# Kernel optimization log

Measured on AMD Instinct MI355X. Metric: run time of the kernel, lower is better.

Reference implementation:

```python
import jax, jax.numpy as jnp
import numpy as np
from jax import lax

T, D, H, O = 16384, 257, 512, 257


def setup_inputs() -> dict:
    key = jax.random.key(0)
    ks = jax.random.split(key, 7)
    s = 1.0 / np.sqrt(H)  # PyTorch LSTM/Linear uniform init scale
    u = lambda k, shp: jax.random.uniform(k, shp, jnp.float32, -s, s)
    return {
        "stft": jax.random.normal(ks[0], (T, D), jnp.float32),
        "W_ih": u(ks[1], (4 * H, D)),
        "W_hh": u(ks[2], (4 * H, H)),
        "b_ih": u(ks[3], (4 * H,)),
        "b_hh": u(ks[4], (4 * H,)),
        "W_out": u(ks[5], (O, H)),
        "b_out": u(ks[6], (O,)),
    }


def reference(stft, W_ih, W_hh, b_ih, b_hh, W_out, b_out):
    # Batch size is 1 (stft.view(T, 1, -1)), so we scan over [T, D] directly.
    # Precompute input-to-gate GEMM for all timesteps: [T, 4H]
    x_gates = stft @ W_ih.T + (b_ih + b_hh)

    def step(carry, xg):
        h, c = carry  # [H], [H]
        g = xg + h @ W_hh.T  # [4H], PyTorch gate order: i, f, g, o
        i, f, gg, o = jnp.split(g, 4)
        i = jax.nn.sigmoid(i)
        f = jax.nn.sigmoid(f)
        gg = jnp.tanh(gg)
        o = jax.nn.sigmoid(o)
        c = f * c + i * gg
        h = o * jnp.tanh(c)
        return (h, c), h

    h0 = jnp.zeros((H,), stft.dtype)  # init_hidden(): zeros
    c0 = jnp.zeros((H,), stft.dtype)
    _, hs = lax.scan(step, (h0, c0), x_gates)  # hs: [T, H]

    out_space = hs @ W_out.T + b_out  # [T, O]
    return jax.nn.log_softmax(out_space, axis=1)
```

## Files before the change

kernel.cpp:

```cpp
#include <hip/hip_runtime.h>
#include <cmath>

#define T_STEPS 16384
#define D_IN    257
#define H_DIM   512
#define O_DIM   257
#define G4      2048

typedef unsigned long long u64;

#define WS_XG_OFF     8192
#define WS_HS_OFF     (8192 + (size_t)T_STEPS * G4 * 4)

__device__ inline float fast_sigmoid(float x) {
    return 1.f / (1.f + __expf(-x));
}
__device__ inline float fast_tanh(float x) {
    float ax = fminf(fabsf(x), 15.f);
    float e  = __expf(2.f * ax);
    float t  = (e - 1.f) / (e + 1.f);
    return copysignf(t, x);
}
__device__ inline float dot4(float4 a, float4 b) {
    return a.x * b.x + a.y * b.y + a.z * b.z + a.w * b.w;
}

#define PIN4(v) asm volatile("" : "+v"(v.x), "+v"(v.y), "+v"(v.z), "+v"(v.w))

__global__ __launch_bounds__(256) void xgate_gemm(
    const float* __restrict__ stft, const float* __restrict__ W_ih,
    const float* __restrict__ b_ih, const float* __restrict__ b_hh,
    float* __restrict__ xg)
{
    const int tid = threadIdx.x;
    const int tx = tid & 15, ty = tid >> 4;
    const int j0 = blockIdx.x * 64;
    const int t0 = blockIdx.y * 64;

    __shared__ float s_a[64][17];
    __shared__ float s_b[64][17];

    float acc[4][4] = {};

    for (int k0 = 0; k0 < D_IN; k0 += 16) {
        #pragma unroll
        for (int l = 0; l < 4; ++l) {
            int idx = tid + l * 256;
            int r  = idx >> 4;
            int kk = idx & 15;
            int k  = k0 + kk;
            s_a[r][kk] = (k < D_IN) ? stft[(size_t)(t0 + r) * D_IN + k] : 0.f;
            s_b[r][kk] = (k < D_IN) ? W_ih[(size_t)(j0 + r) * D_IN + k] : 0.f;
        }
        __syncthreads();
        #pragma unroll
        for (int kk = 0; kk < 16; ++kk) {
            float a[4], b[4];
            #pragma unroll
            for (int r = 0; r < 4; ++r) a[r] = s_a[ty * 4 + r][kk];
            #pragma unroll
            for (int c = 0; c < 4; ++c) b[c] = s_b[tx * 4 + c][kk];
            #pragma unroll
            for (int r = 0; r < 4; ++r)
                #pragma unroll
                for (int c = 0; c < 4; ++c)
                    acc[r][c] += a[r] * b[c];
        }
        __syncthreads();
    }

    float bias[4];
    #pragma unroll
    for (int c = 0; c < 4; ++c) {
        int j = j0 + tx * 4 + c;
        bias[c] = b_ih[j] + b_hh[j];
    }
    #pragma unroll
    for (int r = 0; r < 4; ++r) {
        int t = t0 + ty * 4 + r;
        #pragma unroll
        for (int c = 0; c < 4; ++c) {
            xg[(size_t)t * G4 + j0 + tx * 4 + c] = acc[r][c] + bias[c];
        }
    }
}

__global__ __launch_bounds__(512, 1) void lstm_seq(
    const float* __restrict__ W_hh, const float* __restrict__ xg,
    float* __restrict__ hs, u64* __restrict__ msg)
{
    const int tid  = threadIdx.x;
    const int g    = blockIdx.x;
    const int w    = tid >> 6;
    const int lane = tid & 63;
    const int j    = lane >> 2;
    const int c    = lane & 3;
    const int colb = w * 64 + c * 16;

    const float* wbase = W_hh + (size_t)(g * 16 + j) * H_DIM + colb;
    const size_t gstride = (size_t)H_DIM * H_DIM;
    float4 wA0, wA1, wA2, wA3, wB0, wB1, wB2, wB3;
    float4 wC0, wC1, wC2, wC3, wD0, wD1, wD2, wD3;
    {
        const float4* p0 = (const float4*)(wbase);
        const float4* p1 = (const float4*)(wbase + gstride);
        const float4* p2 = (const float4*)(wbase + 2 * gstride);
        const float4* p3 = (const float4*)(wbase + 3 * gstride);
        wA0 = p0[0]; wA1 = p0[1]; wA2 = p0[2]; wA3 = p0[3];
        wB0 = p1[0]; wB1 = p1[1]; wB2 = p1[2]; wB3 = p1[3];
        wC0 = p2[0]; wC1 = p2[1]; wC2 = p2[2]; wC3 = p2[3];
        wD0 = p3[0]; wD1 = p3[1]; wD2 = p3[2]; wD3 = p3[3];
    }
    PIN4(wA0); PIN4(wA1); PIN4(wA2); PIN4(wA3);
    PIN4(wB0); PIN4(wB1); PIN4(wB2); PIN4(wB3);
    PIN4(wC0); PIN4(wC1); PIN4(wC2); PIN4(wC3);
    PIN4(wD0); PIN4(wD1); PIN4(wD2); PIN4(wD3);

    __shared__ float s_h[512];
    __shared__ float s_part[2][512];

    u64* slot0 = msg;
    u64* slot1 = msg + 512;

    float c_state = 0.f;
    const int t_j = lane & 15;

    for (int t = 0; t < T_STEPS; ++t) {
        const unsigned tagt = (unsigned)t;
        const int buf = t & 1;

        float xv = 0.f;
        if (w == 0)
            xv = __builtin_nontemporal_load(
                xg + (size_t)t * G4 + (lane >> 4) * H_DIM + g * 16 + t_j);

        u64* rp = (buf ? slot1 : slot0) + tid;
        u64 a0 = __hip_atomic_load(rp, __ATOMIC_RELAXED, __HIP_MEMORY_SCOPE_AGENT);
        u64 a1 = __hip_atomic_load(rp, __ATOMIC_RELAXED, __HIP_MEMORY_SCOPE_AGENT);
        u64 a2 = __hip_atomic_load(rp, __ATOMIC_RELAXED, __HIP_MEMORY_SCOPE_AGENT);
        while ((unsigned)(a0 >> 32) != tagt) {
            a0 = a1;
            a1 = a2;
            a2 = __hip_atomic_load(rp, __ATOMIC_RELAXED, __HIP_MEMORY_SCOPE_AGENT);
        }
        const u64 u = a0;

        s_h[tid] = __uint_as_float((unsigned)u);

        const float4* hv = (const float4*)(s_h + colb);
        float4 h0 = hv[0], h1 = hv[1], h2 = hv[2], h3 = hv[3];

        float p0 = dot4(wA0, h0) + dot4(wA1, h1) + dot4(wA2, h2) + dot4(wA3, h3);
        float p1 = dot4(wB0, h0) + dot4(wB1, h1) + dot4(wB2, h2) + dot4(wB3, h3);
        float p2 = dot4(wC0, h0) + dot4(wC1, h1) + dot4(wC2, h2) + dot4(wC3, h3);
        float p3 = dot4(wD0, h0) + dot4(wD1, h1) + dot4(wD2, h2) + dot4(wD3, h3);

        const bool lo2 = (c < 2);
        float a0f = (lo2 ? p0 : p2) + __shfl_xor(lo2 ? p2 : p0, 2, 64);
        float a1f = (lo2 ? p1 : p3) + __shfl_xor(lo2 ? p3 : p1, 2, 64);
        const bool ev = ((c & 1) == 0);
        float fin = (ev ? a0f : a1f) + __shfl_xor(ev ? a1f : a0f, 1, 64);

        s_part[buf][w * 64 + c * 16 + j] = fin;

        asm volatile("s_waitcnt lgkmcnt(0)\n\ts_barrier" ::: "memory");

        if (w == 0) {
            const float* pp = &s_part[buf][0];
            float sum = xv;
            #pragma unroll
            for (int k = 0; k < 8; ++k) sum += pp[k * 64 + lane];

            float gi = __shfl(sum, t_j + 0,  64);
            float gf = __shfl(sum, t_j + 16, 64);
            float gg = __shfl(sum, t_j + 32, 64);
            float go = __shfl(sum, t_j + 48, 64);

            float iv = fast_sigmoid(gi);
            float fv = fast_sigmoid(gf);
            float ov = fast_sigmoid(go);
            float gv = fast_tanh(gg);
            c_state = fv * c_state + iv * gv;
            float hn = ov * fast_tanh(c_state);

            if (lane < 16) {
                __builtin_nontemporal_store(hn, hs + (size_t)t * H_DIM + g * 16 + lane);
                u64 m = ((u64)(tagt + 1) << 32) | (u64)__float_as_uint(hn);
                u64* wp = (((t + 1) & 1) ? slot1 : slot0) + (g * 16 + lane);
                __hip_atomic_store(wp, m, __ATOMIC_RELAXED, __HIP_MEMORY_SCOPE_AGENT);
            }
        }
    }
}

__global__ __launch_bounds__(256) void out_softmax(
    const float* __restrict__ hs, const float* __restrict__ W_out,
    const float* __restrict__ b_out, float* __restrict__ out)
{
    const int tid = threadIdx.x;
    const int t0  = blockIdx.x * 16;

    __shared__ float s_w[257 * 33];
    __shared__ float s_hs[16 * 33];
    __shared__ float s_o[16 * 257];
    __shared__ float s_red[8];

    float acc[16] = {};
    float acc256 = 0.f;

    for (int k0 = 0; k0 < H_DIM; k0 += 32) {
        for (int idx = tid; idx < 257 * 32; idx += 256) {
            int row = idx >> 5, col = idx & 31;
            s_w[row * 33 + col] = W_out[(size_t)row * H_DIM + k0 + col];
        }
        for (int idx = tid; idx < 16 * 32; idx += 256) {
            int row = idx >> 5, col = idx & 31;
            s_hs[row * 33 + col] = hs[(size_t)(t0 + row) * H_DIM + k0 + col];
        }
        __syncthreads();
        #pragma unroll
        for (int kk = 0; kk < 32; ++kk) {
            float w = s_w[tid * 33 + kk];
            #pragma unroll
            for (int r = 0; r < 16; ++r)
                acc[r] += s_hs[r * 33 + kk] * w;
        }
        if (tid < 16) {
            #pragma unroll
            for (int kk = 0; kk < 32; ++kk)
                acc256 += s_w[256 * 33 + kk] * s_hs[tid * 33 + kk];
        }
        __syncthreads();
    }

    float bias_c = b_out[tid];
    #pragma unroll
    for (int r = 0; r < 16; ++r) s_o[r * 257 + tid] = acc[r] + bias_c;
    if (tid < 16) s_o[tid * 257 + 256] = acc256 + b_out[256];
    __syncthreads();

    const int lane = tid & 63, wid = tid >> 6;
    for (int r = 0; r < 16; ++r) {
        float v  = s_o[r * 257 + tid];
        float vx = (tid == 0) ? s_o[r * 257 + 256] : -INFINITY;
        float m = fmaxf(v, vx);
        #pragma unroll
        for (int off = 32; off > 0; off >>= 1) m = fmaxf(m, __shfl_xor(m, off, 64));
        if (lane == 0) s_red[wid] = m;
        __syncthreads();
        m = fmaxf(fmaxf(s_red[0], s_red[1]), fmaxf(s_red[2], s_red[3]));
        float e = expf(v - m) + ((tid == 0) ? expf(vx - m) : 0.f);
        #pragma unroll
        for (int off = 32; off > 0; off >>= 1) e += __shfl_xor(e, off, 64);
        if (lane == 0) s_red[4 + wid] = e;
        __syncthreads();
        float s = s_red[4] + s_red[5] + s_red[6] + s_red[7];
        float lg = logf(s) + m;
        out[(size_t)(t0 + r) * O_DIM + tid] = v - lg;
        if (tid == 0) out[(size_t)(t0 + r) * O_DIM + 256] = vx - lg;
    }
}

extern "C" void kernel_launch(void* const* d_in, const int* in_sizes, int n_in,
                              void* d_out, int out_size, void* d_ws, size_t ws_size,
                              hipStream_t stream) {
    (void)in_sizes; (void)n_in; (void)out_size; (void)ws_size;

    const float* stft  = (const float*)d_in[0];
    const float* W_ih  = (const float*)d_in[1];
    const float* W_hh  = (const float*)d_in[2];
    const float* b_ih  = (const float*)d_in[3];
    const float* b_hh  = (const float*)d_in[4];
    const float* W_out = (const float*)d_in[5];
    const float* b_out = (const float*)d_in[6];
    float* out = (float*)d_out;

    char* ws = (char*)d_ws;
    u64* msg  = (u64*)ws;
    float* xg = (float*)(ws + WS_XG_OFF);
    float* hs = (float*)(ws + WS_HS_OFF);

    (void)hipMemsetAsync(ws, 0, 8192, stream);

    xgate_gemm<<<dim3(G4 / 64, T_STEPS / 64), 256, 0, stream>>>(
        stft, W_ih, b_ih, b_hh, xg);
    lstm_seq<<<32, 512, 0, stream>>>(W_hh, xg, hs, msg);
    out_softmax<<<T_STEPS / 16, 256, 0, stream>>>(hs, W_out, b_out, out);
}
```

Measured before the change: 27.88 ms.

## Co-locate recurrent LSTM blocks on one XCD and exchange state through L2

Launches 256 blocks and uses an XCC-ID election so that 32 blocks on a single XCD take the recurrent roles while the rest exit. Hidden-state messages are then exchanged through that XCD's shared L2 using sc0 loads and stores, which avoids the slower device-scope coherence path on every timestep. A device-scope slow mailbox is still written and polled as a fallback. The scheme relies on at least 32 blocks landing on one XCD at the same time and on the hardware register read; if those assumptions fail it could deadlock, and the fallback costs an extra store per step.

```diff
diff --git a/kernel.cpp b/kernel.cpp
--- a/kernel.cpp
+++ b/kernel.cpp
@@ -9,8 +9,10 @@
 
 typedef unsigned long long u64;
 
-#define WS_XG_OFF     8192
-#define WS_HS_OFF     (8192 + (size_t)T_STEPS * G4 * 4)
+#define WS_SLOW_OFF   8192
+#define WS_ELECT_OFF  16384
+#define WS_XG_OFF     32768
+#define WS_HS_OFF     (32768 + (size_t)T_STEPS * G4 * 4)
 
 __device__ inline float fast_sigmoid(float x) {
     return 1.f / (1.f + __expf(-x));
@@ -26,6 +28,17 @@
 }
 
 #define PIN4(v) asm volatile("" : "+v"(v.x), "+v"(v.y), "+v"(v.z), "+v"(v.w))
+
+__device__ inline u64 ld_l2(const u64* p) {
+    u64 v;
+    asm volatile("global_load_dwordx2 %0, %1, off sc0\n\ts_waitcnt vmcnt(0)"
+                 : "=v"(v) : "v"(p) : "memory");
+    return v;
+}
+__device__ inline void st_l2(u64* p, u64 v) {
+    asm volatile("global_store_dwordx2 %0, %1, off sc0"
+                 :: "v"(p), "v"(v) : "memory");
+}
 
 __global__ __launch_bounds__(256) void xgate_gemm(
     const float* __restrict__ stft, const float* __restrict__ W_ih,
@@ -87,10 +100,35 @@
 
 __global__ __launch_bounds__(512, 1) void lstm_seq(
     const float* __restrict__ W_hh, const float* __restrict__ xg,
-    float* __restrict__ hs, u64* __restrict__ msg)
+    float* __restrict__ hs, u64* __restrict__ fastm, u64* __restrict__ slowm,
+    unsigned* __restrict__ elect)
 {
     const int tid  = threadIdx.x;
-    const int g    = blockIdx.x;
+
+    __shared__ int s_role;
+    if (tid == 0) {
+        unsigned xcc;
+        asm volatile("s_getreg_b32 %0, hwreg(HW_REG_XCC_ID)" : "=s"(xcc));
+        xcc &= 7u;
+        unsigned r = __hip_atomic_fetch_add(&elect[xcc], 1u,
+                                            __ATOMIC_RELAXED, __HIP_MEMORY_SCOPE_AGENT);
+        if (r == 31u) {
+            unsigned expected = 0u;
+            __hip_atomic_compare_exchange_strong(&elect[8], &expected, xcc + 1u,
+                                                 __ATOMIC_RELAXED, __ATOMIC_RELAXED,
+                                                 __HIP_MEMORY_SCOPE_AGENT);
+        }
+        unsigned wxp;
+        do {
+            wxp = __hip_atomic_load(&elect[8], __ATOMIC_RELAXED,
+                                    __HIP_MEMORY_SCOPE_AGENT);
+        } while (wxp == 0u);
+        s_role = (xcc == wxp - 1u && r < 32u) ? (int)r : -1;
+    }
+    __syncthreads();
+    const int g = s_role;
+    if (g < 0) return;
+
     const int w    = tid >> 6;
     const int lane = tid & 63;
     const int j    = lane >> 2;
@@ -119,9 +157,6 @@
     __shared__ float s_h[512];
     __shared__ float s_part[2][512];
 
-    u64* slot0 = msg;
-    u64* slot1 = msg + 512;
-
     float c_state = 0.f;
     const int t_j = lane & 15;
 
@@ -134,16 +169,18 @@
             xv = __builtin_nontemporal_load(
                 xg + (size_t)t * G4 + (lane >> 4) * H_DIM + g * 16 + t_j);
 
-        u64* rp = (buf ? slot1 : slot0) + tid;
-        u64 a0 = __hip_atomic_load(rp, __ATOMIC_RELAXED, __HIP_MEMORY_SCOPE_AGENT);
-        u64 a1 = __hip_atomic_load(rp, __ATOMIC_RELAXED, __HIP_MEMORY_SCOPE_AGENT);
-        u64 a2 = __hip_atomic_load(rp, __ATOMIC_RELAXED, __HIP_MEMORY_SCOPE_AGENT);
-        while ((unsigned)(a0 >> 32) != tagt) {
-            a0 = a1;
-            a1 = a2;
-            a2 = __hip_atomic_load(rp, __ATOMIC_RELAXED, __HIP_MEMORY_SCOPE_AGENT);
-        }
-        const u64 u = a0;
+        u64* fp = fastm + buf * 512 + tid;
+        u64* sp = slowm + buf * 512 + tid;
+        u64 u = ld_l2(fp);
+        int k = 0;
+        while ((unsigned)(u >> 32) != tagt) {
+            if ((++k & 3) == 0) {
+                u64 us = __hip_atomic_load(sp, __ATOMIC_RELAXED,
+                                           __HIP_MEMORY_SCOPE_AGENT);
+                if ((unsigned)(us >> 32) == tagt) { u = us; break; }
+            }
+            u = ld_l2(fp);
+        }
 
         s_h[tid] = __uint_as_float((unsigned)u);
 
@@ -169,7 +206,7 @@
             const float* pp = &s_part[buf][0];
             float sum = xv;
             #pragma unroll
-            for (int k = 0; k < 8; ++k) sum += pp[k * 64 + lane];
+            for (int k2 = 0; k2 < 8; ++k2) sum += pp[k2 * 64 + lane];
 
             float gi = __shfl(sum, t_j + 0,  64);
             float gf = __shfl(sum, t_j + 16, 64);
@@ -186,8 +223,10 @@
             if (lane < 16) {
                 __builtin_nontemporal_store(hn, hs + (size_t)t * H_DIM + g * 16 + lane);
                 u64 m = ((u64)(tagt + 1) << 32) | (u64)__float_as_uint(hn);
-                u64* wp = (((t + 1) & 1) ? slot1 : slot0) + (g * 16 + lane);
-                __hip_atomic_store(wp, m, __ATOMIC_RELAXED, __HIP_MEMORY_SCOPE_AGENT);
+                const int nbuf = (t + 1) & 1;
+                st_l2(fastm + nbuf * 512 + g * 16 + lane, m);
+                __hip_atomic_store(slowm + nbuf * 512 + g * 16 + lane, m,
+                                   __ATOMIC_RELAXED, __HIP_MEMORY_SCOPE_AGENT);
             }
         }
     }
@@ -276,14 +315,16 @@
     float* out = (float*)d_out;
 
     char* ws = (char*)d_ws;
-    u64* msg  = (u64*)ws;
+    u64* fastm = (u64*)ws;
+    u64* slowm = (u64*)(ws + WS_SLOW_OFF);
+    unsigned* elect = (unsigned*)(ws + WS_ELECT_OFF);
     float* xg = (float*)(ws + WS_XG_OFF);
     float* hs = (float*)(ws + WS_HS_OFF);
 
-    (void)hipMemsetAsync(ws, 0, 8192, stream);
+    (void)hipMemsetAsync(ws, 0, 16448, stream);
 
     xgate_gemm<<<dim3(G4 / 64, T_STEPS / 64), 256, 0, stream>>>(
         stft, W_ih, b_ih, b_hh, xg);
-    lstm_seq<<<32, 512, 0, stream>>>(W_hh, xg, hs, msg);
+    lstm_seq<<<256, 512, 0, stream>>>(W_hh, xg, hs, fastm, slowm, elect);
     out_softmax<<<T_STEPS / 16, 256, 0, stream>>>(hs, W_out, b_out, out);
 }
```

After: 33.62 ms. 1.21x slower.
